# Performance work log

Measured on AMD Instinct MI355X. Metric: run time of the kernel, lower is better.

## Reference

```python
import jax, jax.numpy as jnp
import numpy as np

EPS = 1e-12
RANK = 16


def setup_inputs() -> dict:
    key = jax.random.key(0)
    ks = jax.random.split(key, 7)
    bs, seq, d_in, d_out = 8, 2048, 4096, 4096
    n_tasks, n_splits, n_skills, rank = 256, 1, 8, RANK
    return {
        "x": jax.random.normal(ks[0], (bs, seq, d_in), dtype=jnp.float32),
        "task_ids": jax.random.randint(ks[1], (bs,), 0, n_tasks, dtype=jnp.int64 if jax.config.jax_enable_x64 else jnp.int32),
        "weight": jax.random.normal(ks[2], (d_out, d_in), dtype=jnp.float32) * 0.02,
        "bias": jax.random.normal(ks[3], (d_out,), dtype=jnp.float32) * 0.02,
        "module_logits": jax.random.normal(ks[4], (n_tasks, n_splits * n_skills), dtype=jnp.float32) * 0.001,
        "lora_a": jax.random.normal(ks[5], (n_splits, n_skills, d_in // n_splits, rank), dtype=jnp.float32) * 0.01,
        "lora_b": jax.random.normal(ks[6], (n_splits, n_skills, rank, d_out // n_splits), dtype=jnp.float32) * 0.01,
    }


def reference(x, task_ids, weight, bias, module_logits, lora_a, lora_b):
    bs = x.shape[0]
    n_splits, n_skills, _, rank = lora_a.shape
    d_in = n_splits * lora_a.shape[2]
    d_out = n_splits * lora_b.shape[3]
    # PolytroponSelector (eval path): sigmoid then sum-normalize over skills
    logits = module_logits[task_ids].reshape(bs, n_splits, n_skills)
    mw = jax.nn.sigmoid(logits)
    mw = mw / (mw.sum(axis=-1, keepdims=True) + EPS)  # [b, q, s]
    # Mix LoRA skill matrices per example
    A = jnp.einsum('bqs,qsdr->bqdr', mw, lora_a).reshape(bs, d_in, rank)
    B = jnp.einsum('bqs,qsrd->bqrd', mw, lora_b)
    B = jnp.transpose(B, (0, 2, 1, 3)).reshape(bs, rank, d_out)
    adapter_out = jnp.einsum('btr,brd->btd', jnp.einsum('bti,bir->btr', x, A), B) / rank
    base = jnp.einsum('bti,oi->bto', x, weight) + bias
    return base + adapter_out
```

## Files before the change

### kernel.cpp

```cpp
#include <hip/hip_runtime.h>
#include <hip/hip_bf16.h>
#include <cstdint>
#include <cstddef>

typedef __bf16 bf16_t;
typedef __bf16 bf16x8 __attribute__((ext_vector_type(8)));
typedef float f32x4 __attribute__((ext_vector_type(4)));

#define GLP(p)  (const __attribute__((address_space(1))) void*)(p)
#define LDSP(p) (__attribute__((address_space(3))) void*)(p)

static constexpr int BS   = 8;
static constexpr int SEQ  = 2048;
static constexpr int DIN  = 4096;
static constexpr int DOUT = 4096;
static constexpr int NSK  = 8;
static constexpr int RANK = 16;
static constexpr int MTOT = BS * SEQ;

static __device__ __forceinline__ bf16x8 cvt8(float4 v0, float4 v1) {
    bf16x8 o;
    o[0] = (bf16_t)v0.x; o[1] = (bf16_t)v0.y; o[2] = (bf16_t)v0.z; o[3] = (bf16_t)v0.w;
    o[4] = (bf16_t)v1.x; o[5] = (bf16_t)v1.y; o[6] = (bf16_t)v1.z; o[7] = (bf16_t)v1.w;
    return o;
}

__global__ __launch_bounds__(256) void mix_kernel(
    const float* __restrict__ logits, const int* __restrict__ task_ids,
    const float* __restrict__ lora_a, const float* __restrict__ lora_b,
    bf16_t* __restrict__ Abt, bf16_t* __restrict__ Btp) {
    int b = blockIdx.y;
    int c = blockIdx.x;
    int tid = threadIdx.x;

    int t = task_ids[b];
    float w[NSK]; float sum = 0.f;
#pragma unroll
    for (int s = 0; s < NSK; ++s) {
        float lg = logits[t * NSK + s];
        float sg = 1.f / (1.f + __expf(-lg));
        w[s] = sg; sum += sg;
    }
    float inv = 1.f / (sum + 1e-12f);
#pragma unroll
    for (int s = 0; s < NSK; ++s) w[s] *= inv;

    {
        int r = tid & 15, kk = tid >> 4;
#pragma unroll
        for (int i = 0; i < 4; ++i) {
            int k = c * 64 + i * 16 + kk;
            float acc = 0.f;
#pragma unroll
            for (int s = 0; s < NSK; ++s)
                acc += w[s] * lora_a[((size_t)s * DIN + k) * RANK + r];
            Abt[((size_t)b * RANK + r) * DIN + k] = (bf16_t)acc;
        }
    }
    {
        int n = c * 64 + (tid & 63);
        int r0 = tid >> 6;
#pragma unroll
        for (int i = 0; i < 4; ++i) {
            int rr = r0 + i * 4;
            float acc = 0.f;
#pragma unroll
            for (int s = 0; s < NSK; ++s)
                acc += w[s] * lora_b[((size_t)s * RANK + rr) * DOUT + n];
            Btp[((size_t)b * DOUT + n) * 32 + rr] = (bf16_t)acc;
            Btp[((size_t)b * DOUT + n) * 32 + 16 + rr] = (bf16_t)0.f;
        }
    }
}

__global__ __launch_bounds__(256) void convw_kernel(const float* __restrict__ W,
                                                    bf16_t* __restrict__ Wb) {
    size_t g = (size_t)blockIdx.x * 256 + threadIdx.x;
    const float4* src = (const float4*)W;
    float4 v0 = src[g * 2], v1 = src[g * 2 + 1];
    *(bf16x8*)(Wb + g * 8) = cvt8(v0, v1);
}

template<bool XPRE>
__global__ __launch_bounds__(256) void tconv_kernel(
    const float* __restrict__ x, const bf16_t* __restrict__ Abt,
    bf16_t* __restrict__ xb, bf16_t* __restrict__ tpad) {
    __shared__ __align__(16) bf16_t As[64 * 64];
    __shared__ __align__(16) bf16_t Aa[16 * 64];

    int row0 = blockIdx.x * 64;
    int b = row0 >> 11;
    int tid = threadIdx.x;
    int w = tid >> 6, l = tid & 63;
    const bf16_t* Ab = Abt + (size_t)b * RANK * DIN;

    f32x4 acc = {0.f, 0.f, 0.f, 0.f};

    for (int k0 = 0; k0 < DIN; k0 += 64) {
#pragma unroll
        for (int i = 0; i < 2; ++i) {
            int flat = i * 256 + tid;
            int row = flat >> 3, c8 = flat & 7;
            const float* src = x + (size_t)(row0 + row) * DIN + k0 + c8 * 8;
            float4 v0 = *(const float4*)src;
            float4 v1 = *(const float4*)(src + 4);
            bf16x8 o = cvt8(v0, v1);
            *(bf16x8*)(&As[flat * 8]) = o;
            if (XPRE)
                *(bf16x8*)(xb + (size_t)(row0 + row) * DIN + k0 + c8 * 8) = o;
        }
        if (tid < 128) {
            int r = tid >> 3, c8 = tid & 7;
            __builtin_amdgcn_global_load_lds(GLP(Ab + (size_t)r * DIN + k0 + c8 * 8),
                                             LDSP(&Aa[tid * 8]), 16, 0, 0);
        }
        __syncthreads();
#pragma unroll
        for (int s = 0; s < 2; ++s) {
            int kr = s * 32 + (l >> 4) * 8;
            bf16x8 a = *(const bf16x8*)(&As[(w * 16 + (l & 15)) * 64 + kr]);
            bf16x8 bb = *(const bf16x8*)(&Aa[(l & 15) * 64 + kr]);
            acc = __builtin_amdgcn_mfma_f32_16x16x32_bf16(a, bb, acc, 0, 0, 0);
        }
        __syncthreads();
    }
    int r = l & 15;
    int rowb = w * 16 + (l >> 4) * 4;
#pragma unroll
    for (int j = 0; j < 4; ++j) {
        int gm = row0 + rowb + j;
        tpad[(size_t)gm * 32 + r] = (bf16_t)(acc[j] * 0.0625f);
        tpad[(size_t)gm * 32 + 16 + r] = (bf16_t)0.f;
    }
}

#define VMCNT4 asm volatile("s_waitcnt vmcnt(4)" ::: "memory")
#define VMCNT0 asm volatile("s_waitcnt vmcnt(0)" ::: "memory")
#define LGKM0  asm volatile("s_waitcnt lgkmcnt(0)" ::: "memory")
#define SBAR   __builtin_amdgcn_s_barrier()
#define SCHEDB __builtin_amdgcn_sched_barrier(0)

#define MFMA_Q(AREG, BREG, QM, QN)                                             \
    _Pragma("unroll") for (int s_ = 0; s_ < 2; ++s_)                           \
    _Pragma("unroll") for (int i_ = 0; i_ < 4; ++i_)                           \
    _Pragma("unroll") for (int jj_ = 0; jj_ < 2; ++jj_)                        \
        acc[(QM)*4 + i_][(QN)*2 + jj_] =                                       \
            __builtin_amdgcn_mfma_f32_16x16x32_bf16(                           \
                AREG[i_][s_], BREG[jj_][s_], acc[(QM)*4 + i_][(QN)*2 + jj_],   \
                0, 0, 0);

__global__ __launch_bounds__(512, 2) void gemm8_kernel(
    const bf16_t* __restrict__ xb, const bf16_t* __restrict__ Wb,
    const float* __restrict__ bias,
    const bf16_t* __restrict__ tpad, const bf16_t* __restrict__ Btp,
    float* __restrict__ out) {
    __shared__ __align__(16) bf16_t ldsA[2][256 * 64];
    __shared__ __align__(16) bf16_t ldsB[2][256 * 64];

    int tid = threadIdx.x;
    int w = tid >> 6, l = tid & 63;
    int wm = w >> 2, wn = w & 3;
    int l4 = l >> 4, l15 = l & 15;

    int orig = blockIdx.x;
    int id = (orig & 7) * 128 + (orig >> 3);
    int mb = id >> 4, nb = id & 15;
    int row0 = mb * 256, col0 = nb * 256;
    int b = row0 >> 11;

    f32x4 acc[8][4] = {};

    auto stageHalfA = [&](int kt, int c, int h) {
        int k0 = kt * 64;
#pragma unroll
        for (int ld = 0; ld < 2; ++ld) {
            int flat = ld * 512 + tid;
            int r = flat >> 3;
            int sc = (flat & 7) ^ (r & 7);
            __builtin_amdgcn_global_load_lds(
                GLP(xb + (size_t)(row0 + h * 128 + r) * DIN + k0 + sc * 8),
                LDSP(&ldsA[c][h * 8192 + flat * 8]), 16, 0, 0);
        }
    };
    auto stageHalfB = [&](int kt, int c, int h) {
        int k0 = kt * 64;
#pragma unroll
        for (int ld = 0; ld < 2; ++ld) {
            int flat = ld * 512 + tid;
            int r = flat >> 3;
            int sc = (flat & 7) ^ (r & 7);
            __builtin_amdgcn_global_load_lds(
                GLP(Wb + (size_t)(col0 + h * 128 + r) * DIN + k0 + sc * 8),
                LDSP(&ldsB[c][h * 8192 + flat * 8]), 16, 0, 0);
        }
    };
    auto stageAdpA = [&](int c) {
#pragma unroll
        for (int ld = 0; ld < 2; ++ld) {
            int flat = ld * 512 + tid;
            int r = flat >> 2, c4 = flat & 3;
            __builtin_amdgcn_global_load_lds(
                GLP(tpad + (size_t)(row0 + r) * 32 + c4 * 8),
                LDSP(&ldsA[c][flat * 8]), 16, 0, 0);
        }
    };
    auto stageAdpB = [&](int c) {
#pragma unroll
        for (int ld = 0; ld < 2; ++ld) {
            int flat = ld * 512 + tid;
            int r = flat >> 2, c4 = flat & 3;
            __builtin_amdgcn_global_load_lds(
                GLP(Btp + ((size_t)b * DOUT + col0 + r) * 32 + c4 * 8),
                LDSP(&ldsB[c][flat * 8]), 16, 0, 0);
        }
    };

    auto loadA = [&](const bf16_t* base, int QM, bf16x8 (&ar)[4][2]) {
#pragma unroll
        for (int i = 0; i < 4; ++i) {
            int row = QM * 128 + wm * 64 + i * 16 + l15;
#pragma unroll
            for (int s = 0; s < 2; ++s)
                ar[i][s] = *(const bf16x8*)(base + row * 64 +
                                            (((s * 4 + l4) ^ (l15 & 7)) << 3));
        }
    };
    auto loadB = [&](const bf16_t* base, int QN, bf16x8 (&br)[2][2]) {
#pragma unroll
        for (int jj = 0; jj < 2; ++jj) {
            int row = QN * 128 + wn * 32 + jj * 16 + l15;
#pragma unroll
            for (int s = 0; s < 2; ++s)
                br[jj][s] = *(const bf16x8*)(base + row * 64 +
                                             (((s * 4 + l4) ^ (l15 & 7)) << 3));
        }
    };

    stageHalfA(0, 0, 0);
    stageHalfB(0, 0, 0);
    stageHalfB(0, 0, 1);
    stageHalfA(0, 0, 1);
    VMCNT4;
    SCHEDB; SBAR; SCHEDB;

#pragma unroll 1
    for (int j = 0; j < 64; ++j) {
        int c = j & 1, nc = c ^ 1;
        const bf16_t* A_c = &ldsA[c][0];
        const bf16_t* B_c = &ldsB[c][0];
        bf16x8 aA[4][2], aB[4][2], bA[2][2], bB[2][2];

        loadA(A_c, 0, aA);
        loadB(B_c, 0, bA);
        if (j < 63) stageHalfA(j + 1, nc, 0); else stageAdpA(nc);
        VMCNT4; SCHEDB; SBAR;
        LGKM0; SCHEDB;
        __builtin_amdgcn_s_setprio(1);
        MFMA_Q(aA, bA, 0, 0);
        __builtin_amdgcn_s_setprio(0);
        SCHEDB; SBAR;

        loadB(B_c, 1, bB);
        if (j < 63) stageHalfB(j + 1, nc, 0); else stageAdpB(nc);
        VMCNT4; SCHEDB; SBAR;
        LGKM0; SCHEDB;
        __builtin_amdgcn_s_setprio(1);
        MFMA_Q(aA, bB, 0, 1);
        __builtin_amdgcn_s_setprio(0);
        SCHEDB; SBAR;

        loadA(A_c, 1, aB);
        if (j < 63) stageHalfB(j + 1, nc, 1);
        VMCNT4; SCHEDB; SBAR;
        LGKM0; SCHEDB;
        __builtin_amdgcn_s_setprio(1);
        MFMA_Q(aB, bB, 1, 1);
        __builtin_amdgcn_s_setprio(0);
        SCHEDB; SBAR;

        if (j < 63) stageHalfA(j + 1, nc, 1);
        VMCNT4; SCHEDB; SBAR; SCHEDB;
        __builtin_amdgcn_s_setprio(1);
        MFMA_Q(aB, bA, 1, 0);
        __builtin_amdgcn_s_setprio(0);
        SCHEDB; SBAR;
    }

    VMCNT0; SCHEDB; SBAR; SCHEDB;
    {
        const bf16_t* A0 = &ldsA[0][0];
        const bf16_t* B0 = &ldsB[0][0];
        bf16x8 aa[8]; bf16x8 bb[4];
#pragma unroll
        for (int ai = 0; ai < 8; ++ai) {
            int row = (ai >> 2) * 128 + wm * 64 + (ai & 3) * 16 + l15;
            aa[ai] = *(const bf16x8*)(A0 + row * 32 + l4 * 8);
        }
#pragma unroll
        for (int bj = 0; bj < 4; ++bj) {
            int row = (bj >> 1) * 128 + wn * 32 + (bj & 1) * 16 + l15;
            bb[bj] = *(const bf16x8*)(B0 + row * 32 + l4 * 8);
        }
#pragma unroll
        for (int ai = 0; ai < 8; ++ai)
#pragma unroll
            for (int bj = 0; bj < 4; ++bj)
                acc[ai][bj] = __builtin_amdgcn_mfma_f32_16x16x32_bf16(
                    aa[ai], bb[bj], acc[ai][bj], 0, 0, 0);
    }

#pragma unroll
    for (int ai = 0; ai < 8; ++ai) {
        int gm = row0 + (ai >> 2) * 128 + wm * 64 + (ai & 3) * 16 + l4 * 4;
#pragma unroll
        for (int bj = 0; bj < 4; ++bj) {
            int gn = col0 + (bj >> 1) * 128 + wn * 32 + (bj & 1) * 16 + l15;
            float bsv = bias[gn];
#pragma unroll
            for (int q = 0; q < 4; ++q)
                out[(size_t)(gm + q) * DOUT + gn] = acc[ai][bj][q] + bsv;
        }
    }
}

template<bool WPRE>
__global__ __launch_bounds__(256) void gemm_kernel(
    const float* __restrict__ xf,
    const float* __restrict__ Wf, const bf16_t* __restrict__ Wb,
    const float* __restrict__ bias,
    const bf16_t* __restrict__ tpad, const bf16_t* __restrict__ Btp,
    float* __restrict__ out) {
    __shared__ __align__(16) bf16_t As[128 * 64];
    __shared__ __align__(16) bf16_t Bs[128 * 64];

    int orig = blockIdx.x;
    int id = (orig & 7) * 512 + (orig >> 3);
    int mb = id >> 5, nb = id & 31;
    int row0 = mb * 128, col0 = nb * 128;
    int b = row0 >> 11;

    int tid = threadIdx.x;
    int w = tid >> 6, l = tid & 63;
    int wm = w >> 1, wn = w & 1;

    f32x4 acc[4][4] = {};

    for (int k0 = 0; k0 < DIN; k0 += 64) {
#pragma unroll
        for (int i = 0; i < 4; ++i) {
            int flat = i * 256 + tid;
            int row = flat >> 3, c8 = flat & 7;
            const float* src = xf + (size_t)(row0 + row) * DIN + k0 + c8 * 8;
            float4 v0 = *(const float4*)src;
            float4 v1 = *(const float4*)(src + 4);
            *(bf16x8*)(&As[flat * 8]) = cvt8(v0, v1);
        }
        if constexpr (WPRE) {
#pragma unroll
            for (int i = 0; i < 4; ++i) {
                int flat = i * 256 + tid;
                int row = flat >> 3, c8 = flat & 7;
                __builtin_amdgcn_global_load_lds(
                    GLP(Wb + (size_t)(col0 + row) * DIN + k0 + c8 * 8),
                    LDSP(&Bs[flat * 8]), 16, 0, 0);
            }
        } else {
#pragma unroll
            for (int i = 0; i < 4; ++i) {
                int flat = i * 256 + tid;
                int row = flat >> 3, c8 = flat & 7;
                const float* src = Wf + (size_t)(col0 + row) * DIN + k0 + c8 * 8;
                float4 v0 = *(const float4*)src;
                float4 v1 = *(const float4*)(src + 4);
                *(bf16x8*)(&Bs[flat * 8]) = cvt8(v0, v1);
            }
        }
        __syncthreads();
#pragma unroll
        for (int s = 0; s < 2; ++s) {
            int kr = s * 32 + (l >> 4) * 8;
            bf16x8 a[4], bf[4];
#pragma unroll
            for (int i = 0; i < 4; ++i)
                a[i] = *(const bf16x8*)(&As[(wm * 64 + i * 16 + (l & 15)) * 64 + kr]);
#pragma unroll
            for (int j = 0; j < 4; ++j)
                bf[j] = *(const bf16x8*)(&Bs[(wn * 64 + j * 16 + (l & 15)) * 64 + kr]);
#pragma unroll
            for (int i = 0; i < 4; ++i)
#pragma unroll
                for (int j = 0; j < 4; ++j)
                    acc[i][j] = __builtin_amdgcn_mfma_f32_16x16x32_bf16(a[i], bf[j], acc[i][j], 0, 0, 0);
        }
        __syncthreads();
    }

    {
#pragma unroll
        for (int i = 0; i < 2; ++i) {
            int flat = i * 256 + tid;
            int row = flat >> 2, c8 = flat & 3;
            __builtin_amdgcn_global_load_lds(
                GLP(tpad + (size_t)(row0 + row) * 32 + c8 * 8),
                LDSP(&As[flat * 8]), 16, 0, 0);
            __builtin_amdgcn_global_load_lds(
                GLP(Btp + ((size_t)b * DOUT + col0 + row) * 32 + c8 * 8),
                LDSP(&Bs[flat * 8]), 16, 0, 0);
        }
        __syncthreads();
        int kr = (l >> 4) * 8;
        bf16x8 a[4], bf[4];
#pragma unroll
        for (int i = 0; i < 4; ++i)
            a[i] = *(const bf16x8*)(&As[(wm * 64 + i * 16 + (l & 15)) * 32 + kr]);
#pragma unroll
        for (int j = 0; j < 4; ++j)
            bf[j] = *(const bf16x8*)(&Bs[(wn * 64 + j * 16 + (l & 15)) * 32 + kr]);
#pragma unroll
        for (int i = 0; i < 4; ++i)
#pragma unroll
            for (int j = 0; j < 4; ++j)
                acc[i][j] = __builtin_amdgcn_mfma_f32_16x16x32_bf16(a[i], bf[j], acc[i][j], 0, 0, 0);
    }

#pragma unroll
    for (int i = 0; i < 4; ++i) {
        int gm = row0 + wm * 64 + i * 16 + (l >> 4) * 4;
#pragma unroll
        for (int j = 0; j < 4; ++j) {
            int gn = col0 + wn * 64 + j * 16 + (l & 15);
            float bs = bias[gn];
#pragma unroll
            for (int q = 0; q < 4; ++q)
                out[(size_t)(gm + q) * DOUT + gn] = acc[i][j][q] + bs;
        }
    }
}

extern "C" void kernel_launch(void* const* d_in, const int* in_sizes, int n_in,
                              void* d_out, int out_size, void* d_ws, size_t ws_size,
                              hipStream_t stream) {
    const float* x        = (const float*)d_in[0];
    const int*   task_ids = (const int*)d_in[1];
    const float* W        = (const float*)d_in[2];
    const float* bias     = (const float*)d_in[3];
    const float* logits   = (const float*)d_in[4];
    const float* lora_a   = (const float*)d_in[5];
    const float* lora_b   = (const float*)d_in[6];
    float* out = (float*)d_out;

    char* ws = (char*)d_ws;
    size_t off = 0;
    auto alloc = [&](size_t bytes) {
        char* p = ws + off;
        off += (bytes + 255) & ~(size_t)255;
        return p;
    };
    bf16_t* Abt  = (bf16_t*)alloc((size_t)BS * RANK * DIN * 2);
    bf16_t* Btp  = (bf16_t*)alloc((size_t)BS * DOUT * 32 * 2);
    bf16_t* tpad = (bf16_t*)alloc((size_t)MTOT * 32 * 2);
    bf16_t* Wb   = (bf16_t*)alloc((size_t)DOUT * DIN * 2);
    size_t w_end = off;
    bf16_t* xb   = (bf16_t*)alloc((size_t)MTOT * DIN * 2);
    size_t full_end = off;

    bool wpre = ws_size >= w_end;
    bool xpre = ws_size >= full_end;

    mix_kernel<<<dim3(64, 8), 256, 0, stream>>>(logits, task_ids, lora_a, lora_b, Abt, Btp);
    if (wpre)
        convw_kernel<<<(DOUT * DIN / 8) / 256, 256, 0, stream>>>(W, Wb);
    if (xpre)
        tconv_kernel<true><<<MTOT / 64, 256, 0, stream>>>(x, Abt, xb, tpad);
    else
        tconv_kernel<false><<<MTOT / 64, 256, 0, stream>>>(x, Abt, nullptr, tpad);

    if (xpre) {
        int nblk = (MTOT / 256) * (DOUT / 256);
        gemm8_kernel<<<nblk, 512, 0, stream>>>(xb, Wb, bias, tpad, Btp, out);
    } else {
        int nblk = (MTOT / 128) * (DOUT / 128);
        if (wpre)
            gemm_kernel<true><<<nblk, 256, 0, stream>>>(x, W, Wb, bias, tpad, Btp, out);
        else
            gemm_kernel<false><<<nblk, 256, 0, stream>>>(x, W, Wb, bias, tpad, Btp, out);
    }
}
```

Measured before the change: 699.4 us.

## Deepen GEMM global-to-LDS prefetch to two K-tiles ahead

Restructures the main bf16 GEMM loop so the global_load_lds prefetch runs two K-tiles ahead instead of one. The LDS is split into per-quadrant buffers, the last two tiles are peeled, and the vmcnt waits are retuned for the deeper pipeline. The aim is to hide more global memory latency behind the MFMA work. Correctness now depends on the hand-counted vmcnt values, and the stores issued after the main loop have a different timing.

```diff
diff --git a/kernel.cpp b/kernel.cpp
--- a/kernel.cpp
+++ b/kernel.cpp
@@ -134,11 +134,12 @@
     }
 }
 
-#define VMCNT4 asm volatile("s_waitcnt vmcnt(4)" ::: "memory")
-#define VMCNT0 asm volatile("s_waitcnt vmcnt(0)" ::: "memory")
 #define LGKM0  asm volatile("s_waitcnt lgkmcnt(0)" ::: "memory")
 #define SBAR   __builtin_amdgcn_s_barrier()
 #define SCHEDB __builtin_amdgcn_sched_barrier(0)
+#define PRIO1  __builtin_amdgcn_s_setprio(1)
+#define PRIO0  __builtin_amdgcn_s_setprio(0)
+#define VMG(TXT) asm volatile("s_waitcnt " TXT ::: "memory")
 
 #define MFMA_Q(AREG, BREG, QM, QN)                                             \
     _Pragma("unroll") for (int s_ = 0; s_ < 2; ++s_)                           \
@@ -149,13 +150,43 @@
                 AREG[i_][s_], BREG[jj_][s_], acc[(QM)*4 + i_][(QN)*2 + jj_],   \
                 0, 0, 0);
 
+#define TILE_BODY(CP, ISS1, ISS2, ISS3, G0TXT, G1TXT, G3TXT)                   \
+  {                                                                            \
+    const bf16_t* A0s = &lds[CP][0][0];                                        \
+    const bf16_t* A1s = &lds[CP][1][0];                                        \
+    const bf16_t* B0s = &lds[CP][2][0];                                        \
+    const bf16_t* B1s = &lds[CP][3][0];                                        \
+    bf16x8 aA[4][2], aB[4][2], bA[2][2], bB[2][2];                             \
+                                                 \
+    loadA(A0s, aA); loadB(B0s, bA);                                            \
+    SCHEDB; SBAR; LGKM0; SCHEDB;                                               \
+    PRIO1; MFMA_Q(aA, bA, 0, 0); PRIO0;                                        \
+    VMG(G0TXT); SCHEDB; SBAR; SCHEDB;                                          \
+                                                 \
+    loadB(B1s, bB);                                                            \
+    ISS1;                                                                      \
+    SCHEDB; SBAR; LGKM0; SCHEDB;                                               \
+    PRIO1; MFMA_Q(aA, bB, 0, 1); PRIO0;                                        \
+    VMG(G1TXT); SCHEDB; SBAR; SCHEDB;                                          \
+                                                 \
+    loadA(A1s, aB);                                                            \
+    ISS2;                                                                      \
+    SCHEDB; SBAR; LGKM0; SCHEDB;                                               \
+    PRIO1; MFMA_Q(aB, bB, 1, 1); PRIO0;                                        \
+    SCHEDB; SBAR; SCHEDB;                                                      \
+                                                 \
+    ISS3;                                                                      \
+    SCHEDB; SBAR; SCHEDB;                                                      \
+    PRIO1; MFMA_Q(aB, bA, 1, 0); PRIO0;                                        \
+    VMG(G3TXT); SCHEDB; SBAR; SCHEDB;                                          \
+  }
+
 __global__ __launch_bounds__(512, 2) void gemm8_kernel(
     const bf16_t* __restrict__ xb, const bf16_t* __restrict__ Wb,
     const float* __restrict__ bias,
     const bf16_t* __restrict__ tpad, const bf16_t* __restrict__ Btp,
     float* __restrict__ out) {
-    __shared__ __align__(16) bf16_t ldsA[2][256 * 64];
-    __shared__ __align__(16) bf16_t ldsB[2][256 * 64];
+    __shared__ __align__(16) bf16_t lds[2][4][128 * 64];
 
     int tid = threadIdx.x;
     int w = tid >> 6, l = tid & 63;
@@ -170,65 +201,69 @@
 
     f32x4 acc[8][4] = {};
 
-    auto stageHalfA = [&](int kt, int c, int h) {
+    auto stageA = [&](int kt, int par, int half) {
         int k0 = kt * 64;
+        const bf16_t* src = xb + (size_t)(row0 + half * 128) * DIN;
+        bf16_t* dst = &lds[par][half][0];
 #pragma unroll
         for (int ld = 0; ld < 2; ++ld) {
             int flat = ld * 512 + tid;
             int r = flat >> 3;
             int sc = (flat & 7) ^ (r & 7);
             __builtin_amdgcn_global_load_lds(
-                GLP(xb + (size_t)(row0 + h * 128 + r) * DIN + k0 + sc * 8),
-                LDSP(&ldsA[c][h * 8192 + flat * 8]), 16, 0, 0);
-        }
-    };
-    auto stageHalfB = [&](int kt, int c, int h) {
+                GLP(src + (size_t)r * DIN + k0 + sc * 8),
+                LDSP(dst + flat * 8), 16, 0, 0);
+        }
+    };
+    auto stageB = [&](int kt, int par, int half) {
         int k0 = kt * 64;
+        const bf16_t* src = Wb + (size_t)(col0 + half * 128) * DIN;
+        bf16_t* dst = &lds[par][2 + half][0];
 #pragma unroll
         for (int ld = 0; ld < 2; ++ld) {
             int flat = ld * 512 + tid;
             int r = flat >> 3;
             int sc = (flat & 7) ^ (r & 7);
             __builtin_amdgcn_global_load_lds(
-                GLP(Wb + (size_t)(col0 + h * 128 + r) * DIN + k0 + sc * 8),
-                LDSP(&ldsB[c][h * 8192 + flat * 8]), 16, 0, 0);
-        }
-    };
-    auto stageAdpA = [&](int c) {
+                GLP(src + (size_t)r * DIN + k0 + sc * 8),
+                LDSP(dst + flat * 8), 16, 0, 0);
+        }
+    };
+    auto stageAdpA = [&]() {
 #pragma unroll
         for (int ld = 0; ld < 2; ++ld) {
             int flat = ld * 512 + tid;
             int r = flat >> 2, c4 = flat & 3;
             __builtin_amdgcn_global_load_lds(
                 GLP(tpad + (size_t)(row0 + r) * 32 + c4 * 8),
-                LDSP(&ldsA[c][flat * 8]), 16, 0, 0);
-        }
-    };
-    auto stageAdpB = [&](int c) {
+                LDSP(&lds[0][0][flat * 8]), 16, 0, 0);
+        }
+    };
+    auto stageAdpB = [&]() {
 #pragma unroll
         for (int ld = 0; ld < 2; ++ld) {
             int flat = ld * 512 + tid;
             int r = flat >> 2, c4 = flat & 3;
             __builtin_amdgcn_global_load_lds(
                 GLP(Btp + ((size_t)b * DOUT + col0 + r) * 32 + c4 * 8),
-                LDSP(&ldsB[c][flat * 8]), 16, 0, 0);
-        }
-    };
-
-    auto loadA = [&](const bf16_t* base, int QM, bf16x8 (&ar)[4][2]) {
+                LDSP(&lds[0][2][flat * 8]), 16, 0, 0);
+        }
+    };
+
+    auto loadA = [&](const bf16_t* base, bf16x8 (&ar)[4][2]) {
 #pragma unroll
         for (int i = 0; i < 4; ++i) {
-            int row = QM * 128 + wm * 64 + i * 16 + l15;
+            int row = wm * 64 + i * 16 + l15;
 #pragma unroll
             for (int s = 0; s < 2; ++s)
                 ar[i][s] = *(const bf16x8*)(base + row * 64 +
                                             (((s * 4 + l4) ^ (l15 & 7)) << 3));
         }
     };
-    auto loadB = [&](const bf16_t* base, int QN, bf16x8 (&br)[2][2]) {
+    auto loadB = [&](const bf16_t* base, bf16x8 (&br)[2][2]) {
 #pragma unroll
         for (int jj = 0; jj < 2; ++jj) {
-            int row = QN * 128 + wn * 32 + jj * 16 + l15;
+            int row = wn * 32 + jj * 16 + l15;
 #pragma unroll
             for (int s = 0; s < 2; ++s)
                 br[jj][s] = *(const bf16x8*)(base + row * 64 +
@@ -236,60 +271,31 @@
         }
     };
 
-    stageHalfA(0, 0, 0);
-    stageHalfB(0, 0, 0);
-    stageHalfB(0, 0, 1);
-    stageHalfA(0, 0, 1);
-    VMCNT4;
+    stageA(0, 0, 0); stageB(0, 0, 0); stageB(0, 0, 1); stageA(0, 0, 1);
+    stageA(1, 1, 0); stageB(1, 1, 0); stageB(1, 1, 1); stageA(1, 1, 1);
+    VMG("vmcnt(12)");
     SCHEDB; SBAR; SCHEDB;
 
 #pragma unroll 1
-    for (int j = 0; j < 64; ++j) {
-        int c = j & 1, nc = c ^ 1;
-        const bf16_t* A_c = &ldsA[c][0];
-        const bf16_t* B_c = &ldsB[c][0];
-        bf16x8 aA[4][2], aB[4][2], bA[2][2], bB[2][2];
-
-        loadA(A_c, 0, aA);
-        loadB(B_c, 0, bA);
-        if (j < 63) stageHalfA(j + 1, nc, 0); else stageAdpA(nc);
-        VMCNT4; SCHEDB; SBAR;
-        LGKM0; SCHEDB;
-        __builtin_amdgcn_s_setprio(1);
-        MFMA_Q(aA, bA, 0, 0);
-        __builtin_amdgcn_s_setprio(0);
-        SCHEDB; SBAR;
-
-        loadB(B_c, 1, bB);
-        if (j < 63) stageHalfB(j + 1, nc, 0); else stageAdpB(nc);
-        VMCNT4; SCHEDB; SBAR;
-        LGKM0; SCHEDB;
-        __builtin_amdgcn_s_setprio(1);
-        MFMA_Q(aA, bB, 0, 1);
-        __builtin_amdgcn_s_setprio(0);
-        SCHEDB; SBAR;
-
-        loadA(A_c, 1, aB);
-        if (j < 63) stageHalfB(j + 1, nc, 1);
-        VMCNT4; SCHEDB; SBAR;
-        LGKM0; SCHEDB;
-        __builtin_amdgcn_s_setprio(1);
-        MFMA_Q(aB, bB, 1, 1);
-        __builtin_amdgcn_s_setprio(0);
-        SCHEDB; SBAR;
-
-        if (j < 63) stageHalfA(j + 1, nc, 1);
-        VMCNT4; SCHEDB; SBAR; SCHEDB;
-        __builtin_amdgcn_s_setprio(1);
-        MFMA_Q(aB, bA, 1, 0);
-        __builtin_amdgcn_s_setprio(0);
-        SCHEDB; SBAR;
-    }
-
-    VMCNT0; SCHEDB; SBAR; SCHEDB;
+    for (int j = 0; j < 62; ++j) {
+        int cp = j & 1;
+        TILE_BODY(cp,
+                  { stageA(j + 2, cp, 0); stageB(j + 2, cp, 0); },
+                  { stageB(j + 2, cp, 1); },
+                  { stageA(j + 2, cp, 1); },
+                  "vmcnt(10)", "vmcnt(12)", "vmcnt(12)");
+    }
+    TILE_BODY(0,
+              { stageAdpA(); stageAdpB(); },
+              {}, {},
+              "vmcnt(10)", "vmcnt(12)", "vmcnt(8)");
+    TILE_BODY(1,
+              {}, {}, {},
+              "vmcnt(6)", "vmcnt(4)", "vmcnt(0)");
+
     {
-        const bf16_t* A0 = &ldsA[0][0];
-        const bf16_t* B0 = &ldsB[0][0];
+        const bf16_t* A0 = &lds[0][0][0];
+        const bf16_t* B0 = &lds[0][2][0];
         bf16x8 aa[8]; bf16x8 bb[4];
 #pragma unroll
         for (int ai = 0; ai < 8; ++ai) {
```

After: 611.8 us. -12.5%, faster.
